# Performance work log

Measured on AMD Instinct MI355X. Metric: run time of the kernel, lower is better.

The kernel has to match this reference:

```python
import jax, jax.numpy as jnp
import numpy as np

B, L, D_MODEL, H, MAX_DIST = 4, 1024, 1024, 16, 64
DEPTH = D_MODEL // H
VOCAB = 2 * MAX_DIST + 1


def setup_inputs() -> dict:
    key = jax.random.key(0)
    ks = jax.random.split(key, 12)
    s = 0.02
    return {
        "x": jax.random.normal(ks[0], (B, L, D_MODEL), jnp.float32),
        "mask": jnp.zeros((B, 1, 1, L), jnp.float32),
        "wq": jax.random.normal(ks[1], (D_MODEL, D_MODEL), jnp.float32) * s,
        "bq": jnp.zeros((D_MODEL,), jnp.float32),
        "wk": jax.random.normal(ks[2], (D_MODEL, D_MODEL), jnp.float32) * s,
        "bk": jnp.zeros((D_MODEL,), jnp.float32),
        "wv": jax.random.normal(ks[3], (D_MODEL, D_MODEL), jnp.float32) * s,
        "bv": jnp.zeros((D_MODEL,), jnp.float32),
        "wo": jax.random.normal(ks[4], (D_MODEL, D_MODEL), jnp.float32) * s,
        "bo": jnp.zeros((D_MODEL,), jnp.float32),
        "rel_k_table": jax.random.normal(ks[5], (VOCAB, DEPTH), jnp.float32) * s,
        "rel_v_table": jax.random.normal(ks[6], (VOCAB, DEPTH), jnp.float32) * s,
    }


def _split_heads(t):
    # [B, L, d_model] -> [B, H, L, depth]
    return t.reshape(B, L, H, DEPTH).transpose(0, 2, 1, 3)


def reference(x, mask, wq, bq, wk, bk, wv, bv, wo, bo, rel_k_table, rel_v_table):
    # q/k/v projections (self-attention)
    q = _split_heads(x @ wq + bq)
    k = _split_heads(x @ wk + bk)
    v = _split_heads(x @ wv + bv)

    # relative positions matrix [L, L], clipped to [-MAX_DIST, MAX_DIST] then shifted
    r = jnp.arange(L)
    rel_mat = jnp.clip(r[None, :] - r[:, None], -MAX_DIST, MAX_DIST) + MAX_DIST
    rel_k = rel_k_table[rel_mat]  # [L, L, depth]
    rel_v = rel_v_table[rel_mat]  # [L, L, depth]

    # _relative_attention_inner(q, k, rel_k, transpose=True):
    # logits = q k^T + q . rel_k  (note: t2t relative path applies no 1/sqrt(dk) scale)
    logits = (jnp.einsum('bhqd,bhkd->bhqk', q, k)
              + jnp.einsum('bhqd,qkd->bhqk', q, rel_k))
    logits = logits + mask * (-1e9)  # bias
    weights = jax.nn.softmax(logits, axis=-1)  # [B, H, L, L]

    # _relative_attention_inner(weights, v, rel_v, transpose=False)
    ctx = (jnp.einsum('bhqk,bhkd->bhqd', weights, v)
           + jnp.einsum('bhqk,qkd->bhqd', weights, rel_v))

    # combine heads and output projection
    ctx = ctx.transpose(0, 2, 1, 3).reshape(B, L, D_MODEL)
    out = ctx @ wo + bo
    return out
```

## Files before the change

kernel.cpp:

```cpp
#include <hip/hip_runtime.h>
#include <hip/hip_bf16.h>
#include <cstdint>
#include <cstddef>

typedef unsigned int u32;
typedef __attribute__((ext_vector_type(8))) short s16x8;
typedef __attribute__((ext_vector_type(4))) short s16x4;
typedef __attribute__((ext_vector_type(4))) float f32x4;
typedef __attribute__((ext_vector_type(2))) u32   u32x2;

#define MFMA(a,b,c) __builtin_amdgcn_mfma_f32_16x16x32_bf16(a,b,c,0,0,0)

#if __has_builtin(__builtin_amdgcn_mfma_f32_16x16x16bf16_1k)
#define MFMA16(a,b,c) __builtin_amdgcn_mfma_f32_16x16x16bf16_1k(a,b,c,0,0,0)
#else
static __device__ __forceinline__ f32x4 MFMA16(s16x4 a, s16x4 b, f32x4 c){
    f32x4 d;
    asm("v_mfma_f32_16x16x16_bf16 %0, %1, %2, %3"
        : "=v"(d) : "v"(a), "v"(b), "v"(c));
    return d;
}
#endif

__device__ __forceinline__ short f2bf(float f) {
    u32 u = __builtin_bit_cast(u32, f);
    u32 r = (u + 0x7fffu + ((u >> 16) & 1u)) >> 16;
    return (short)r;
}
__device__ __forceinline__ float bf2f(short s) {
    return __builtin_bit_cast(float, ((u32)(unsigned short)s) << 16);
}
__device__ __forceinline__ u32 cvtpk(float lo, float hi) {
    u32 r;
    asm("v_cvt_pk_bf16_f32 %0, %1, %2" : "=v"(r) : "v"(lo), "v"(hi));
    return r;
}
__device__ __forceinline__ void async_copy16(void* lds, const void* g) {
    __builtin_amdgcn_global_load_lds((const __attribute__((address_space(1))) u32*)g,
                                     (__attribute__((address_space(3))) u32*)lds, 16, 0, 0);
}

__global__ __launch_bounds__(256)
void prep_all(const float* __restrict__ x, short* __restrict__ xb,
              const float* __restrict__ wq, const float* __restrict__ wk,
              const float* __restrict__ wv, const float* __restrict__ wo,
              short* __restrict__ Wtqkv, short* __restrict__ Wto,
              const float* __restrict__ relk, const float* __restrict__ relv,
              short* __restrict__ relkb, short* __restrict__ relvT,
              const float* __restrict__ mask, short* __restrict__ maskPb)
{
    __shared__ float sT[64][68];
    const int bid = blockIdx.x;
    const int tid = threadIdx.x;

    if (bid < 2048) {
        int i = (bid * 256 + tid) * 8;
        float4 a = *(const float4*)&x[i];
        float4 b = *(const float4*)&x[i + 4];
        s16x8 v = { f2bf(a.x), f2bf(a.y), f2bf(a.z), f2bf(a.w),
                    f2bf(b.x), f2bf(b.y), f2bf(b.z), f2bf(b.w) };
        *(s16x8*)&xb[i] = v;
    } else if (bid < 3072) {
        const int wid = bid - 2048;
        const int kt = wid & 15, nt = (wid >> 4) & 15, seg = wid >> 8;
        const float* src = seg == 0 ? wq : seg == 1 ? wk : seg == 2 ? wv : wo;
        const int k0 = kt * 64, n0 = nt * 64;
#pragma unroll
        for (int i = 0; i < 4; ++i) {
            int t2 = tid + i * 256;
            int r = t2 >> 4, c4 = t2 & 15;
            *(float4*)&sT[r][c4 * 4] = *(const float4*)&src[(size_t)(k0 + r) * 1024 + n0 + c4 * 4];
        }
        __syncthreads();
#pragma unroll
        for (int i = 0; i < 2; ++i) {
            int t2 = tid + i * 256;
            int rn = t2 >> 3, ch = t2 & 7;
            s16x8 v;
#pragma unroll
            for (int j = 0; j < 8; ++j) v[j] = f2bf(sT[ch * 8 + j][rn]);
            if (seg < 3)
                *(s16x8*)&Wtqkv[(size_t)(seg * 1024 + n0 + rn) * 1024 + k0 + ch * 8] = v;
            else
                *(s16x8*)&Wto[(size_t)(n0 + rn) * 1024 + k0 + ch * 8] = v;
        }
    } else {
        int gt = (bid - 3072) * 256 + tid;
        for (int i = gt; i < 144 * 64; i += 256 * 8) {
            int r = i >> 6, d = i & 63;
            relkb[i] = (r < 129) ? f2bf(relk[r * 64 + d]) : (short)0;
        }
        for (int i = gt; i < 64 * 128; i += 256 * 8) {
            int d = i >> 7, r = i & 127;
            relvT[i] = f2bf(relv[r * 64 + d]);
        }
        for (int i = gt; i < 4096; i += 256 * 8)
            maskPb[i] = f2bf(mask[i] * -1e9f);
    }
}

__global__ __launch_bounds__(256, 4)
void gemm_qkv(const short* __restrict__ Ab, const short* __restrict__ Wt,
              const float* __restrict__ bq, const float* __restrict__ bk,
              const float* __restrict__ bv,
              short* __restrict__ Qb, short* __restrict__ Kb, short* __restrict__ Vtb)
{
    __shared__ __align__(16) short As[128 * 64];
    __shared__ __align__(16) short Bs[128 * 64];
    const int tid = threadIdx.x;
    const int w = tid >> 6, lane = tid & 63;
    const int lo16 = lane & 15, hi = lane >> 4;
    const int pb = blockIdx.x;
    const int wg = (pb & 7) * 96 + (pb >> 3);
    const int n0g = (wg % 24) * 128;
    const int m0 = (wg / 24) * 128;
    const int wr = w >> 1, wc = w & 1;

    f32x4 acc[4][4] = {};

    for (int t = 0; t < 16; ++t) {
        const int k0 = t * 64;
        __syncthreads();
#pragma unroll
        for (int i = 0; i < 4; ++i) {
            int o = i * 4096 + tid * 16;
            int row = o >> 7;
            int cb = o & 127;
            int sc = cb ^ ((row & 7) << 4);
            async_copy16((char*)As + o, Ab + (size_t)(m0 + row) * 1024 + k0 + (sc >> 1));
            async_copy16((char*)Bs + o, Wt + (size_t)(n0g + row) * 1024 + k0 + (sc >> 1));
        }
        __syncthreads();
#pragma unroll
        for (int ks = 0; ks < 2; ++ks) {
            s16x8 aF[4], bF[4];
#pragma unroll
            for (int mi = 0; mi < 4; ++mi) {
                int row = wr * 64 + mi * 16 + lo16;
                int cb = ks * 64 + hi * 16;
                aF[mi] = *(const s16x8*)((const char*)As + row * 128 + (cb ^ ((row & 7) << 4)));
            }
#pragma unroll
            for (int ni = 0; ni < 4; ++ni) {
                int row = wc * 64 + ni * 16 + lo16;
                int cb = ks * 64 + hi * 16;
                bF[ni] = *(const s16x8*)((const char*)Bs + row * 128 + (cb ^ ((row & 7) << 4)));
            }
#pragma unroll
            for (int mi = 0; mi < 4; ++mi)
#pragma unroll
                for (int ni = 0; ni < 4; ++ni)
                    acc[mi][ni] = MFMA(aF[mi], bF[ni], acc[mi][ni]);
        }
    }

    const int seg = n0g >> 10;
    const int nn = n0g & 1023;
    const float* bias = seg == 0 ? bq : seg == 1 ? bk : bv;
    float bv4[4];
#pragma unroll
    for (int ni = 0; ni < 4; ++ni) bv4[ni] = bias[nn + wc * 64 + ni * 16 + lo16];

    if (seg == 2) {
#pragma unroll
        for (int mi = 0; mi < 4; ++mi)
#pragma unroll
            for (int ni = 0; ni < 4; ++ni) {
                int nl = nn + wc * 64 + ni * 16 + lo16;
                int hh = nl >> 6, d = nl & 63;
                int mbase = m0 + wr * 64 + mi * 16 + hi * 4;
                int bb = mbase >> 10, l0 = mbase & 1023;
                int j0 = l0 & 31;
                int col = (l0 >> 5) * 32 + (((j0 >> 4) & 1) << 2) + (((j0 >> 2) & 3) << 3);
                s16x4 pk = { f2bf(acc[mi][ni][0] + bv4[ni]),
                             f2bf(acc[mi][ni][1] + bv4[ni]),
                             f2bf(acc[mi][ni][2] + bv4[ni]),
                             f2bf(acc[mi][ni][3] + bv4[ni]) };
                *(s16x4*)&Vtb[((size_t)(bb * 16 + hh) * 64 + d) * 1024 + col] = pk;
            }
    } else {
        short* out = seg == 0 ? Qb : Kb;
#pragma unroll
        for (int mi = 0; mi < 4; ++mi)
#pragma unroll
            for (int ni = 0; ni < 4; ++ni) {
                int nl = nn + wc * 64 + ni * 16 + lo16;
                int hh = nl >> 6, d = nl & 63;
#pragma unroll
                for (int r = 0; r < 4; ++r) {
                    int m = m0 + wr * 64 + mi * 16 + hi * 4 + r;
                    int bb = m >> 10, l = m & 1023;
                    out[(((size_t)bb * 16 + hh) * 1024 + l) * 64 + d] = f2bf(acc[mi][ni][r] + bv4[ni]);
                }
            }
    }
}

__global__ __launch_bounds__(256, 4)
void attn_mfma(const short* __restrict__ Qb, const short* __restrict__ Kb,
               const short* __restrict__ Vtb, const short* __restrict__ relkb,
               const short* __restrict__ relvTb, const float* __restrict__ relv_f32,
               const short* __restrict__ maskPb, short* __restrict__ CTXb)
{
    __shared__ __align__(16) short sK[32 * 64];
    __shared__ __align__(16) short sV[64 * 32];
    __shared__ __align__(16) short sQrel[4][16][128];
    __shared__ __align__(16) short sBand[4][16][128];

    const int tid = threadIdx.x;
    const int w = tid >> 6, lane = tid & 63;
    const int lo16 = lane & 15, hi = lane >> 4;
    const int qsw = (lo16 & 7) << 4;
    const int vm = (lo16 >> 1) & 3;

    const int p = blockIdx.x;
    const int bid = (p & 7) * 128 + (p >> 3);
    const int bh = bid >> 4;
    const int qt = bid & 15;
    const int b = bh >> 4, h = bh & 15;
    const int q0 = qt * 64 + w * 16;
    const int q_abs = q0 + lo16;

    const short* Kbase = Kb + (size_t)bh * 65536;
    const short* Vtbase = Vtb + (size_t)bh * 65536;
    const short* mbase = maskPb + b * 1024;

    const int skr = tid >> 3, skc = tid & 7;
    const int svd = tid >> 2, svc = tid & 3;
    const short* ksrc = Kbase + (size_t)skr * 64 + ((skc ^ (skr & 7)) << 3);
    const short* vsrc = Vtbase + (size_t)svd * 1024 + ((svc ^ ((svd >> 1) & 3)) << 3);

    async_copy16((char*)&sK[0] + tid * 16, ksrc);
    async_copy16((char*)&sV[0] + tid * 16, vsrc);

    const short* qptr = Qb + ((size_t)bh * 1024 + q_abs) * 64 + hi * 8;
    const s16x8 qB0 = *(const s16x8*)qptr;
    const s16x8 qB1 = *(const s16x8*)(qptr + 32);

    {
        u32* bz = (u32*)&sBand[w][0][0];
#pragma unroll
        for (int i = 0; i < 16; ++i) bz[lane + i * 64] = 0u;
    }

    f32x4 dq8 = {0.f, 0.f, 0.f, 0.f};
#pragma unroll
    for (int rf = 0; rf < 9; ++rf) {
        const short* rp = relkb + (size_t)(rf * 16 + lo16) * 64 + hi * 8;
        s16x8 rA0 = *(const s16x8*)rp;
        s16x8 rA1 = *(const s16x8*)(rp + 32);
        f32x4 dq = {0.f, 0.f, 0.f, 0.f};
        dq = MFMA(rA0, qB0, dq);
        dq = MFMA(rA1, qB1, dq);
        if (rf < 8) {
            s16x4 pk = { f2bf(dq[0]), f2bf(dq[1]), f2bf(dq[2]), f2bf(dq[3]) };
            *(s16x4*)&sQrel[w][lo16][(rf * 16 + hi * 4) ^ qsw] = pk;
        } else {
            dq8 = dq;
        }
    }
    const float qrel_lo = bf2f(sQrel[w][lo16][0 ^ qsw]);
    const float qrel_hi = __shfl(bf2f(f2bf(dq8[0])), lo16);

    __syncthreads();

    f32x4 ctx[4] = {};
    float lsum = 0.f, lov = 0.f, hiv = 0.f;
    const f32x4 z = {0.f, 0.f, 0.f, 0.f};
    const int km = lo16 & 7;

    for (int t = 0; t < 32; ++t) {
        const int kf = t * 32;
        s16x8 kr0 = *(const s16x8*)(sK + lo16 * 64 + ((hi ^ km) << 3));
        s16x8 kr1 = *(const s16x8*)(sK + lo16 * 64 + (((hi + 4) ^ km) << 3));
        s16x8 kr2 = *(const s16x8*)(sK + (lo16 + 16) * 64 + ((hi ^ km) << 3));
        s16x8 kr3 = *(const s16x8*)(sK + (lo16 + 16) * 64 + (((hi + 4) ^ km) << 3));
        s16x8 vr0 = *(const s16x8*)(sV + lo16 * 32 + ((hi ^ vm) << 3));
        s16x8 vr1 = *(const s16x8*)(sV + (16 + lo16) * 32 + ((hi ^ vm) << 3));
        s16x8 vr2 = *(const s16x8*)(sV + (32 + lo16) * 32 + ((hi ^ vm) << 3));
        s16x8 vr3 = *(const s16x8*)(sV + (48 + lo16) * 32 + ((hi ^ vm) << 3));
        s16x4 m0 = *(const s16x4*)&mbase[kf + hi * 4];
        s16x4 m1 = *(const s16x4*)&mbase[kf + 16 + hi * 4];
        __syncthreads();
        const int kfn = ((t + 1) & 31) * 32;
        async_copy16((char*)&sK[0] + tid * 16, ksrc + (size_t)kfn * 64);
        async_copy16((char*)&sV[0] + tid * 16, vsrc + kfn);

        __builtin_amdgcn_s_setprio(1);
        f32x4 s0 = MFMA(kr0, qB0, z);
        f32x4 s1 = MFMA(kr2, qB0, z);
        s0 = MFMA(kr1, qB1, s0);
        s1 = MFMA(kr3, qB1, s1);
        __builtin_amdgcn_s_setprio(0);

        float pr[8];
        if (kf + 95 <= q0 || kf >= q0 + 79) {
            const float qc = (kf < q0) ? qrel_lo : qrel_hi;
            float bs = 0.f;
#pragma unroll
            for (int r = 0; r < 4; ++r) {
                pr[r]     = __expf(s0[r] + qc + bf2f(m0[r]));
                pr[4 + r] = __expf(s1[r] + qc + bf2f(m1[r]));
            }
#pragma unroll
            for (int r = 0; r < 8; ++r) bs += pr[r];
            lsum += bs;
            if (kf < q0) lov += bs; else hiv += bs;
        } else {
#pragma unroll
            for (int f = 0; f < 2; ++f)
#pragma unroll
                for (int r = 0; r < 4; ++r) {
                    int k_abs = kf + f * 16 + hi * 4 + r;
                    int dd = k_abs - q_abs;
                    dd = dd < -64 ? -64 : (dd > 64 ? 64 : dd);
                    int rel = dd + 64;
                    int relc = rel > 127 ? 127 : rel;
                    float qv = bf2f(sQrel[w][lo16][relc ^ qsw]);
                    if (rel == 128) qv = qrel_hi;
                    float sv = f ? s1[r] : s0[r];
                    float mv = bf2f(f ? m1[r] : m0[r]);
                    float pex = __expf(sv + qv + mv);
                    pr[f * 4 + r] = pex;
                    lsum += pex;
                    if (rel >= 1 && rel <= 127) sBand[w][lo16][rel ^ qsw] = f2bf(pex);
                    else if (rel == 0) lov += pex;
                    else hiv += pex;
                }
        }
        u32x2 w0 = { cvtpk(pr[0], pr[1]), cvtpk(pr[2], pr[3]) };
        u32x2 w1 = { cvtpk(pr[4], pr[5]), cvtpk(pr[6], pr[7]) };
        s16x4 pf0 = __builtin_bit_cast(s16x4, w0);
        s16x4 pf1 = __builtin_bit_cast(s16x4, w1);

        s16x4 a0 = __builtin_shufflevector(vr0, vr0, 0, 1, 2, 3);
        s16x4 b0 = __builtin_shufflevector(vr0, vr0, 4, 5, 6, 7);
        s16x4 a1 = __builtin_shufflevector(vr1, vr1, 0, 1, 2, 3);
        s16x4 b1 = __builtin_shufflevector(vr1, vr1, 4, 5, 6, 7);
        s16x4 a2 = __builtin_shufflevector(vr2, vr2, 0, 1, 2, 3);
        s16x4 b2 = __builtin_shufflevector(vr2, vr2, 4, 5, 6, 7);
        s16x4 a3 = __builtin_shufflevector(vr3, vr3, 0, 1, 2, 3);
        s16x4 b3 = __builtin_shufflevector(vr3, vr3, 4, 5, 6, 7);
        __builtin_amdgcn_s_setprio(1);
        ctx[0] = MFMA16(a0, pf0, ctx[0]);
        ctx[1] = MFMA16(a1, pf0, ctx[1]);
        ctx[2] = MFMA16(a2, pf0, ctx[2]);
        ctx[3] = MFMA16(a3, pf0, ctx[3]);
        ctx[0] = MFMA16(b0, pf1, ctx[0]);
        ctx[1] = MFMA16(b1, pf1, ctx[1]);
        ctx[2] = MFMA16(b2, pf1, ctx[2]);
        ctx[3] = MFMA16(b3, pf1, ctx[3]);
        __builtin_amdgcn_s_setprio(0);

        __syncthreads();
    }

#pragma unroll
    for (int ks = 0; ks < 4; ++ks) {
        s16x8 bB = *(const s16x8*)&sBand[w][lo16][(ks * 32 + hi * 8) ^ qsw];
#pragma unroll
        for (int df = 0; df < 4; ++df) {
            s16x8 rA = *(const s16x8*)(relvTb + (size_t)(df * 16 + lo16) * 128 + ks * 32 + hi * 8);
            ctx[df] = MFMA(rA, bB, ctx[df]);
        }
    }

    lsum += __shfl_xor(lsum, 16); lsum += __shfl_xor(lsum, 32);
    lov  += __shfl_xor(lov, 16);  lov  += __shfl_xor(lov, 32);
    hiv  += __shfl_xor(hiv, 16);  hiv  += __shfl_xor(hiv, 32);
    const float inv = 1.0f / lsum;

#pragma unroll
    for (int df = 0; df < 4; ++df) {
        s16x4 pk;
#pragma unroll
        for (int r = 0; r < 4; ++r) {
            int d = df * 16 + hi * 4 + r;
            float t = ctx[df][r] + lov * relv_f32[d] + hiv * relv_f32[128 * 64 + d];
            pk[r] = f2bf(t * inv);
        }
        *(s16x4*)(CTXb + ((size_t)(b * 1024) + q_abs) * 1024 + h * 64 + df * 16 + hi * 4) = pk;
    }
}

__global__ __launch_bounds__(256, 4)
void gemm_out(const short* __restrict__ Ab, const short* __restrict__ Wto,
              const float* __restrict__ bo, float* __restrict__ out)
{
    __shared__ __align__(16) short As[128 * 64];
    __shared__ __align__(16) short Bs[64 * 64];
    const int tid = threadIdx.x;
    const int w = tid >> 6, lane = tid & 63;
    const int lo16 = lane & 15, hi = lane >> 4;
    const int pb = blockIdx.x;
    const int wg = (pb & 7) * 64 + (pb >> 3);
    const int n0 = (wg & 15) * 64;
    const int m0 = (wg >> 4) * 128;
    const int wr = w;

    f32x4 acc[2][4] = {};

    for (int t = 0; t < 16; ++t) {
        const int k0 = t * 64;
        __syncthreads();
#pragma unroll
        for (int i = 0; i < 4; ++i) {
            int o = i * 4096 + tid * 16;
            int row = o >> 7;
            int cb = o & 127;
            int sc = cb ^ ((row & 7) << 4);
            async_copy16((char*)As + o, Ab + (size_t)(m0 + row) * 1024 + k0 + (sc >> 1));
        }
#pragma unroll
        for (int i = 0; i < 2; ++i) {
            int o = i * 4096 + tid * 16;
            int row = o >> 7;
            int cb = o & 127;
            int sc = cb ^ ((row & 7) << 4);
            async_copy16((char*)Bs + o, Wto + (size_t)(n0 + row) * 1024 + k0 + (sc >> 1));
        }
        __syncthreads();
#pragma unroll
        for (int ks = 0; ks < 2; ++ks) {
            s16x8 aF[2], bF[4];
#pragma unroll
            for (int mi = 0; mi < 2; ++mi) {
                int row = wr * 32 + mi * 16 + lo16;
                int cb = ks * 64 + hi * 16;
                aF[mi] = *(const s16x8*)((const char*)As + row * 128 + (cb ^ ((row & 7) << 4)));
            }
#pragma unroll
            for (int ni = 0; ni < 4; ++ni) {
                int row = ni * 16 + lo16;
                int cb = ks * 64 + hi * 16;
                bF[ni] = *(const s16x8*)((const char*)Bs + row * 128 + (cb ^ ((row & 7) << 4)));
            }
#pragma unroll
            for (int mi = 0; mi < 2; ++mi)
#pragma unroll
                for (int ni = 0; ni < 4; ++ni)
                    acc[mi][ni] = MFMA(aF[mi], bF[ni], acc[mi][ni]);
        }
    }

    float bv4[4];
#pragma unroll
    for (int ni = 0; ni < 4; ++ni) bv4[ni] = bo[n0 + ni * 16 + lo16];
#pragma unroll
    for (int mi = 0; mi < 2; ++mi)
#pragma unroll
        for (int ni = 0; ni < 4; ++ni)
#pragma unroll
            for (int r = 0; r < 4; ++r) {
                int m = m0 + wr * 32 + mi * 16 + hi * 4 + r;
                out[(size_t)m * 1024 + n0 + ni * 16 + lo16] = acc[mi][ni][r] + bv4[ni];
            }
}

extern "C" void kernel_launch(void* const* d_in, const int* in_sizes, int n_in,
                              void* d_out, int out_size, void* d_ws, size_t ws_size,
                              hipStream_t stream)
{
    (void)in_sizes; (void)n_in; (void)out_size; (void)ws_size;
    const float* x    = (const float*)d_in[0];
    const float* mask = (const float*)d_in[1];
    const float* wq   = (const float*)d_in[2];
    const float* bq   = (const float*)d_in[3];
    const float* wk   = (const float*)d_in[4];
    const float* bk   = (const float*)d_in[5];
    const float* wv   = (const float*)d_in[6];
    const float* bv   = (const float*)d_in[7];
    const float* wo   = (const float*)d_in[8];
    const float* bo   = (const float*)d_in[9];
    const float* relk = (const float*)d_in[10];
    const float* relv = (const float*)d_in[11];
    float* out = (float*)d_out;

    char* p = (char*)d_ws;
    short* xb     = (short*)p; p += (size_t)4096 * 1024 * 2;
    short* Wtqkv  = (short*)p; p += (size_t)3072 * 1024 * 2;
    short* Wto    = (short*)p; p += (size_t)1024 * 1024 * 2;
    short* Qb     = (short*)p; p += (size_t)4096 * 1024 * 2;
    short* Kb     = (short*)p; p += (size_t)4096 * 1024 * 2;
    short* Vtb    = (short*)p; p += (size_t)4096 * 1024 * 2;
    short* CTXb   = (short*)p; p += (size_t)4096 * 1024 * 2;
    short* relkb  = (short*)p; p += (size_t)144 * 64 * 2;
    short* relvT  = (short*)p; p += (size_t)64 * 128 * 2;
    short* maskPb = (short*)p; p += (size_t)4096 * 2;

    prep_all  <<<3080, 256, 0, stream>>>(x, xb, wq, wk, wv, wo, Wtqkv, Wto,
                                         relk, relv, relkb, relvT, mask, maskPb);
    gemm_qkv  <<<768, 256, 0, stream>>>(xb, Wtqkv, bq, bk, bv, Qb, Kb, Vtb);
    attn_mfma <<<1024, 256, 0, stream>>>(Qb, Kb, Vtb, relkb, relvT, relv, maskPb, CTXb);
    gemm_out  <<<512, 256, 0, stream>>>(CTXb, Wto, bo, out);
}
```

Baseline: 114.1 us.

## Double-buffer K/V tiles, merge Qrel/band LDS, and use exp2 with prescaled Q

Double-buffers the K and V shared-memory tiles so the async copy of the next tile is issued before the current one is consumed, removing one barrier per iteration. The Qrel and band-probability LDS arrays are merged into one buffer that is overwritten in place, with edge entries zeroed after the loop for the first and last query tiles. Q and the mask bias are prescaled by log2(e) so the softmax can use the native exp2 instruction instead of expf. This lowers LDS use, which may raise occupancy, but adds fix-up logic for the boundary entries that must be correct for the first and last tiles.

```diff
diff --git a/kernel.cpp b/kernel.cpp
--- a/kernel.cpp
+++ b/kernel.cpp
@@ -21,6 +21,12 @@
     return d;
 }
 #endif
+
+#define LOG2E 1.4426950408889634f
+
+__device__ __forceinline__ float fexp2(float x) {
+    return __builtin_amdgcn_exp2f(x);
+}
 
 __device__ __forceinline__ short f2bf(float f) {
     u32 u = __builtin_bit_cast(u32, f);
@@ -95,7 +101,7 @@
             relvT[i] = f2bf(relv[r * 64 + d]);
         }
         for (int i = gt; i < 4096; i += 256 * 8)
-            maskPb[i] = f2bf(mask[i] * -1e9f);
+            maskPb[i] = f2bf(mask[i] * (-1e9f * LOG2E));
     }
 }
 
@@ -157,6 +163,7 @@
     const int seg = n0g >> 10;
     const int nn = n0g & 1023;
     const float* bias = seg == 0 ? bq : seg == 1 ? bk : bv;
+    const float oscale = (seg == 0) ? LOG2E : 1.0f;
     float bv4[4];
 #pragma unroll
     for (int ni = 0; ni < 4; ++ni) bv4[ni] = bias[nn + wc * 64 + ni * 16 + lo16];
@@ -190,7 +197,8 @@
                 for (int r = 0; r < 4; ++r) {
                     int m = m0 + wr * 64 + mi * 16 + hi * 4 + r;
                     int bb = m >> 10, l = m & 1023;
-                    out[(((size_t)bb * 16 + hh) * 1024 + l) * 64 + d] = f2bf(acc[mi][ni][r] + bv4[ni]);
+                    out[(((size_t)bb * 16 + hh) * 1024 + l) * 64 + d] =
+                        f2bf((acc[mi][ni][r] + bv4[ni]) * oscale);
                 }
             }
     }
@@ -202,10 +210,9 @@
                const short* __restrict__ relvTb, const float* __restrict__ relv_f32,
                const short* __restrict__ maskPb, short* __restrict__ CTXb)
 {
-    __shared__ __align__(16) short sK[32 * 64];
-    __shared__ __align__(16) short sV[64 * 32];
-    __shared__ __align__(16) short sQrel[4][16][128];
-    __shared__ __align__(16) short sBand[4][16][128];
+    __shared__ __align__(16) short sK[2][32 * 64];
+    __shared__ __align__(16) short sV[2][64 * 32];
+    __shared__ __align__(16) short sQB[4][16][128];
 
     const int tid = threadIdx.x;
     const int w = tid >> 6, lane = tid & 63;
@@ -230,18 +237,12 @@
     const short* ksrc = Kbase + (size_t)skr * 64 + ((skc ^ (skr & 7)) << 3);
     const short* vsrc = Vtbase + (size_t)svd * 1024 + ((svc ^ ((svd >> 1) & 3)) << 3);
 
-    async_copy16((char*)&sK[0] + tid * 16, ksrc);
-    async_copy16((char*)&sV[0] + tid * 16, vsrc);
+    async_copy16((char*)&sK[0][0] + tid * 16, ksrc);
+    async_copy16((char*)&sV[0][0] + tid * 16, vsrc);
 
     const short* qptr = Qb + ((size_t)bh * 1024 + q_abs) * 64 + hi * 8;
     const s16x8 qB0 = *(const s16x8*)qptr;
     const s16x8 qB1 = *(const s16x8*)(qptr + 32);
-
-    {
-        u32* bz = (u32*)&sBand[w][0][0];
-#pragma unroll
-        for (int i = 0; i < 16; ++i) bz[lane + i * 64] = 0u;
-    }
 
     f32x4 dq8 = {0.f, 0.f, 0.f, 0.f};
 #pragma unroll
@@ -254,12 +255,12 @@
         dq = MFMA(rA1, qB1, dq);
         if (rf < 8) {
             s16x4 pk = { f2bf(dq[0]), f2bf(dq[1]), f2bf(dq[2]), f2bf(dq[3]) };
-            *(s16x4*)&sQrel[w][lo16][(rf * 16 + hi * 4) ^ qsw] = pk;
+            *(s16x4*)&sQB[w][lo16][(rf * 16 + hi * 4) ^ qsw] = pk;
         } else {
             dq8 = dq;
         }
     }
-    const float qrel_lo = bf2f(sQrel[w][lo16][0 ^ qsw]);
+    const float qrel_lo = bf2f(sQB[w][lo16][0 ^ qsw]);
     const float qrel_hi = __shfl(bf2f(f2bf(dq8[0])), lo16);
 
     __syncthreads();
@@ -271,20 +272,20 @@
 
     for (int t = 0; t < 32; ++t) {
         const int kf = t * 32;
-        s16x8 kr0 = *(const s16x8*)(sK + lo16 * 64 + ((hi ^ km) << 3));
-        s16x8 kr1 = *(const s16x8*)(sK + lo16 * 64 + (((hi + 4) ^ km) << 3));
-        s16x8 kr2 = *(const s16x8*)(sK + (lo16 + 16) * 64 + ((hi ^ km) << 3));
-        s16x8 kr3 = *(const s16x8*)(sK + (lo16 + 16) * 64 + (((hi + 4) ^ km) << 3));
-        s16x8 vr0 = *(const s16x8*)(sV + lo16 * 32 + ((hi ^ vm) << 3));
-        s16x8 vr1 = *(const s16x8*)(sV + (16 + lo16) * 32 + ((hi ^ vm) << 3));
-        s16x8 vr2 = *(const s16x8*)(sV + (32 + lo16) * 32 + ((hi ^ vm) << 3));
-        s16x8 vr3 = *(const s16x8*)(sV + (48 + lo16) * 32 + ((hi ^ vm) << 3));
+        const int cur = t & 1, nxt = (t + 1) & 1;
+        const int kfn = ((t + 1) & 31) * 32;
+        async_copy16((char*)&sK[nxt][0] + tid * 16, ksrc + (size_t)kfn * 64);
+        async_copy16((char*)&sV[nxt][0] + tid * 16, vsrc + kfn);
+        s16x8 kr0 = *(const s16x8*)(sK[cur] + lo16 * 64 + ((hi ^ km) << 3));
+        s16x8 kr1 = *(const s16x8*)(sK[cur] + lo16 * 64 + (((hi + 4) ^ km) << 3));
+        s16x8 kr2 = *(const s16x8*)(sK[cur] + (lo16 + 16) * 64 + ((hi ^ km) << 3));
+        s16x8 kr3 = *(const s16x8*)(sK[cur] + (lo16 + 16) * 64 + (((hi + 4) ^ km) << 3));
+        s16x8 vr0 = *(const s16x8*)(sV[cur] + lo16 * 32 + ((hi ^ vm) << 3));
+        s16x8 vr1 = *(const s16x8*)(sV[cur] + (16 + lo16) * 32 + ((hi ^ vm) << 3));
+        s16x8 vr2 = *(const s16x8*)(sV[cur] + (32 + lo16) * 32 + ((hi ^ vm) << 3));
+        s16x8 vr3 = *(const s16x8*)(sV[cur] + (48 + lo16) * 32 + ((hi ^ vm) << 3));
         s16x4 m0 = *(const s16x4*)&mbase[kf + hi * 4];
         s16x4 m1 = *(const s16x4*)&mbase[kf + 16 + hi * 4];
-        __syncthreads();
-        const int kfn = ((t + 1) & 31) * 32;
-        async_copy16((char*)&sK[0] + tid * 16, ksrc + (size_t)kfn * 64);
-        async_copy16((char*)&sV[0] + tid * 16, vsrc + kfn);
 
         __builtin_amdgcn_s_setprio(1);
         f32x4 s0 = MFMA(kr0, qB0, z);
@@ -299,8 +300,8 @@
             float bs = 0.f;
 #pragma unroll
             for (int r = 0; r < 4; ++r) {
-                pr[r]     = __expf(s0[r] + qc + bf2f(m0[r]));
-                pr[4 + r] = __expf(s1[r] + qc + bf2f(m1[r]));
+                pr[r]     = fexp2(s0[r] + qc + bf2f(m0[r]));
+                pr[4 + r] = fexp2(s1[r] + qc + bf2f(m1[r]));
             }
 #pragma unroll
             for (int r = 0; r < 8; ++r) bs += pr[r];
@@ -316,14 +317,14 @@
                     dd = dd < -64 ? -64 : (dd > 64 ? 64 : dd);
                     int rel = dd + 64;
                     int relc = rel > 127 ? 127 : rel;
-                    float qv = bf2f(sQrel[w][lo16][relc ^ qsw]);
+                    float qv = bf2f(sQB[w][lo16][relc ^ qsw]);
                     if (rel == 128) qv = qrel_hi;
                     float sv = f ? s1[r] : s0[r];
                     float mv = bf2f(f ? m1[r] : m0[r]);
-                    float pex = __expf(sv + qv + mv);
+                    float pex = fexp2(sv + qv + mv);
                     pr[f * 4 + r] = pex;
                     lsum += pex;
-                    if (rel >= 1 && rel <= 127) sBand[w][lo16][rel ^ qsw] = f2bf(pex);
+                    if (rel >= 1 && rel <= 127) sQB[w][lo16][rel ^ qsw] = f2bf(pex);
                     else if (rel == 0) lov += pex;
                     else hiv += pex;
                 }
@@ -355,9 +356,21 @@
         __syncthreads();
     }
 
+    if (hi == 0) {
+        sQB[w][lo16][0 ^ qsw] = 0;
+        if (qt == 0) {
+            for (int rel = 1; rel <= 63 - q_abs; ++rel)
+                sQB[w][lo16][rel ^ qsw] = 0;
+        } else if (qt == 15) {
+            for (int rel = 1088 - q_abs; rel <= 127; ++rel)
+                sQB[w][lo16][rel ^ qsw] = 0;
+        }
+    }
+    __syncthreads();
+
 #pragma unroll
     for (int ks = 0; ks < 4; ++ks) {
-        s16x8 bB = *(const s16x8*)&sBand[w][lo16][(ks * 32 + hi * 8) ^ qsw];
+        s16x8 bB = *(const s16x8*)&sQB[w][lo16][(ks * 32 + hi * 8) ^ qsw];
 #pragma unroll
         for (int df = 0; df < 4; ++df) {
             s16x8 rA = *(const s16x8*)(relvTb + (size_t)(df * 16 + lo16) * 128 + ks * 32 + hi * 8);
```

After: 115.0 us. No clear change (+0.8%).
